# Performance work log

Measured on AMD Instinct MI355X. Metric: run time of the kernel, lower is better.

Reference implementation:

```python
import jax, jax.numpy as jnp
import numpy as np

OBS_DIM, ACT_DIM = 512, 32
H1, H2 = 1024, 1024
BATCH = 4096
LOG2PI = float(np.log(2.0 * np.pi))


def setup_inputs() -> dict:
    key = jax.random.key(0)
    ks = jax.random.split(key, 9)
    def uinit(k, shape, fan_in):
        b = 1.0 / np.sqrt(fan_in)
        return jax.random.uniform(k, shape, jnp.float32, -b, b)
    return {
        "obs": jax.random.normal(ks[0], (BATCH, OBS_DIM), jnp.float32),
        "act": jax.random.normal(ks[1], (BATCH, ACT_DIM), jnp.float32),
        # stacked per-head weights: [act_dim, in, out]
        "W1": uinit(ks[2], (ACT_DIM, OBS_DIM, H1), OBS_DIM),
        "b1": uinit(ks[3], (ACT_DIM, H1), OBS_DIM),
        "W2": uinit(ks[4], (ACT_DIM, H1, H2), H1),
        "b2": uinit(ks[5], (ACT_DIM, H2), H1),
        "W3": uinit(ks[6], (ACT_DIM, H2), H2),   # out dim 1, squeezed
        "b3": uinit(ks[7], (ACT_DIM,), H2),
        "log_std": jnp.full((ACT_DIM,), -0.5, jnp.float32),
    }


def reference(obs, act, W1, b1, W2, b2, W3, b3, log_std):
    # act_dim decoupled 3-layer MLPs as batched GEMMs over the head axis 'a'
    x = jnp.tanh(jnp.einsum('bo,aoh->bah', obs, W1) + b1)          # [B, A, H1]
    x = jnp.tanh(jnp.einsum('bah,ahk->bak', x, W2) + b2)           # [B, A, H2]
    mu = jnp.einsum('bak,ak->ba', x, W3) + b3                      # [B, A]
    # diagonal Normal log_prob(act).sum(-1)
    z = (act - mu) * jnp.exp(-log_std)
    logp = jnp.sum(-0.5 * (z * z + LOG2PI) - log_std, axis=-1)     # [B]
    return (mu, logp)
```

## Files before the change

### kernel.cpp

```cpp
#include <hip/hip_runtime.h>
#include <hip/hip_bf16.h>

typedef unsigned short u16;
typedef __bf16 bf16x8 __attribute__((ext_vector_type(8)));
typedef float f32x4 __attribute__((ext_vector_type(4)));

#define LOG2PI_F 1.8378770664093453f

__device__ __forceinline__ u16 f2bf(float f) {
  union { __hip_bfloat16 h; u16 u; } cvt;
  cvt.h = __float2bfloat16(f);
  return cvt.u;
}

__device__ __forceinline__ float fast_tanh(float x) {
  float e = __expf(2.0f * x);
  return 1.0f - 2.0f * __builtin_amdgcn_rcpf(e + 1.0f);
}

__device__ __forceinline__ void load_lds16(const void* g, void* l) {
  __builtin_amdgcn_global_load_lds(
      (const __attribute__((address_space(1))) void*)g,
      (__attribute__((address_space(3))) void*)l,
      16, 0, 0);
}

__global__ void cvt_f32_bf16(const float* __restrict__ in, u16* __restrict__ out, int n4) {
  int i = blockIdx.x * blockDim.x + threadIdx.x;
  int stride = gridDim.x * blockDim.x;
  for (int j = i; j < n4; j += stride) {
    float4 v = reinterpret_cast<const float4*>(in)[j];
    ushort4 o;
    o.x = f2bf(v.x); o.y = f2bf(v.y); o.z = f2bf(v.z); o.w = f2bf(v.w);
    reinterpret_cast<ushort4*>(out)[j] = o;
  }
}

__global__ void transpose_cvt(const float* __restrict__ W, u16* __restrict__ Wt,
                              int K, int N) {
  __shared__ u16 t[64][66];
  const int a = blockIdx.z;
  const int n0 = blockIdx.x * 64, k0 = blockIdx.y * 64;
  const float* Wh = W + (size_t)a * K * N;
  u16* Wth = Wt + (size_t)a * N * K;
  const int tid = threadIdx.x;
#pragma unroll
  for (int j = 0; j < 16; ++j) {
    int idx = j * 256 + tid;
    int r = idx >> 6, c = idx & 63;
    t[r][c] = f2bf(Wh[(size_t)(k0 + r) * N + n0 + c]);
  }
  __syncthreads();
#pragma unroll
  for (int j = 0; j < 16; ++j) {
    int idx = j * 256 + tid;
    int r = idx >> 6, c = idx & 63;
    Wth[(size_t)(n0 + r) * K + k0 + c] = t[c][r];
  }
}

template <int MODE>
__global__ __launch_bounds__(256, 2) void gemm_heads(
    const u16* __restrict__ A, long aHeadStride,
    const u16* __restrict__ Bt,
    const float* __restrict__ bias,
    int M, int N, int K, int gridN,
    u16* __restrict__ outBf,
    const float* __restrict__ W3,
    float* __restrict__ muAcc) {
  __shared__ __align__(16) u16 As[128 * 64];
  __shared__ __align__(16) u16 Bs[128 * 64];

  const int tid = threadIdx.x;
  const int l = tid & 63;
  const int w = tid >> 6;
  const int wm = w >> 1, wn = w & 1;
  const int lh = l & 15, lg = l >> 4;

  const int cpx = gridDim.x >> 3;
  const int bid = (blockIdx.x & 7) * cpx + (blockIdx.x >> 3);
  const int bph = (M >> 7) * gridN;
  const int head = bid / bph;
  const int rem = bid % bph;
  const int m0 = (rem / gridN) << 7;
  const int n0 = (rem % gridN) << 7;

  const u16* Ah = A + (size_t)head * (size_t)aHeadStride;
  const u16* Bh = Bt + (size_t)head * (size_t)N * (size_t)K;

  f32x4 acc[4][4] = {};

  for (int kt = 0; kt < K; kt += 64) {
#pragma unroll
    for (int i = 0; i < 4; ++i) {
      const int c = i * 256 + tid;
      const int row = c >> 3, j = c & 7;
      const int js = j ^ (row & 7);
      load_lds16(Ah + (size_t)(m0 + row) * K + kt + js * 8, &As[c * 8]);
    }
#pragma unroll
    for (int i = 0; i < 4; ++i) {
      const int c = i * 256 + tid;
      const int row = c >> 3, j = c & 7;
      const int js = j ^ (row & 7);
      load_lds16(Bh + (size_t)(n0 + row) * K + kt + js * 8, &Bs[c * 8]);
    }
    __syncthreads();

#pragma unroll
    for (int ks = 0; ks < 2; ++ks) {
      bf16x8 af[4], bfr[4];
#pragma unroll
      for (int mf = 0; mf < 4; ++mf) {
        const int row = wm * 64 + mf * 16 + lh;
        const int j = (ks * 4 + lg) ^ (lh & 7);
        af[mf] = *reinterpret_cast<const bf16x8*>(&As[row * 64 + j * 8]);
      }
#pragma unroll
      for (int nf = 0; nf < 4; ++nf) {
        const int row = wn * 64 + nf * 16 + lh;
        const int j = (ks * 4 + lg) ^ (lh & 7);
        bfr[nf] = *reinterpret_cast<const bf16x8*>(&Bs[row * 64 + j * 8]);
      }
#pragma unroll
      for (int mf = 0; mf < 4; ++mf)
#pragma unroll
        for (int nf = 0; nf < 4; ++nf)
          acc[mf][nf] = __builtin_amdgcn_mfma_f32_16x16x32_bf16(
              af[mf], bfr[nf], acc[mf][nf], 0, 0, 0);
    }
    __syncthreads();
  }

  if (MODE == 1) {
    u16* Oh = outBf + (size_t)head * (size_t)M * (size_t)N;
#pragma unroll
    for (int mf = 0; mf < 4; ++mf) {
#pragma unroll
      for (int r = 0; r < 4; ++r) {
        const int row = m0 + wm * 64 + mf * 16 + lg * 4 + r;
#pragma unroll
        for (int nf = 0; nf < 4; ++nf) {
          const int col = n0 + wn * 64 + nf * 16 + lh;
          float v = acc[mf][nf][r] + bias[head * N + col];
          Oh[(size_t)row * N + col] = f2bf(fast_tanh(v));
        }
      }
    }
  } else {
#pragma unroll
    for (int mf = 0; mf < 4; ++mf) {
#pragma unroll
      for (int r = 0; r < 4; ++r) {
        const int row = m0 + wm * 64 + mf * 16 + lg * 4 + r;
        float p = 0.f;
#pragma unroll
        for (int nf = 0; nf < 4; ++nf) {
          const int col = n0 + wn * 64 + nf * 16 + lh;
          float v = acc[mf][nf][r] + bias[head * N + col];
          p += fast_tanh(v) * W3[head * N + col];
        }
        p += __shfl_xor(p, 1);
        p += __shfl_xor(p, 2);
        p += __shfl_xor(p, 4);
        p += __shfl_xor(p, 8);
        if (lh == 0) atomicAdd(&muAcc[(size_t)row * 32 + head], p);
      }
    }
  }
}

__global__ void finalize_kernel(const float* __restrict__ muAcc,
                                const float* __restrict__ b3,
                                const float* __restrict__ lstd,
                                const float* __restrict__ act,
                                float* __restrict__ out, int M) {
  int b = blockIdx.x * 256 + threadIdx.x;
  if (b >= M) return;
  float lp = 0.f;
#pragma unroll
  for (int a = 0; a < 32; ++a) {
    float mu = muAcc[(size_t)b * 32 + a] + b3[a];
    out[(size_t)b * 32 + a] = mu;
    float ls = lstd[a];
    float z = (act[(size_t)b * 32 + a] - mu) * __expf(-ls);
    lp += -0.5f * (z * z + LOG2PI_F) - ls;
  }
  out[(size_t)M * 32 + b] = lp;
}

extern "C" void kernel_launch(void* const* d_in, const int* in_sizes, int n_in,
                              void* d_out, int out_size, void* d_ws, size_t ws_size,
                              hipStream_t stream) {
  const float* obs = (const float*)d_in[0];
  const float* act = (const float*)d_in[1];
  const float* W1 = (const float*)d_in[2];
  const float* b1 = (const float*)d_in[3];
  const float* W2 = (const float*)d_in[4];
  const float* b2 = (const float*)d_in[5];
  const float* W3 = (const float*)d_in[6];
  const float* b3 = (const float*)d_in[7];
  const float* lstd = (const float*)d_in[8];

  constexpr int B = 4096, OBS = 512, A = 32, H1 = 1024, H2 = 1024;

  u16* obs_bf = (u16*)d_ws;
  u16* W1t = obs_bf + (size_t)B * OBS;
  u16* W2t = W1t + (size_t)A * H1 * OBS;
  u16* x1 = W2t + (size_t)A * H2 * H1;
  float* muAcc = (float*)(x1 + (size_t)A * B * H1);
  float* out = (float*)d_out;

  hipMemsetAsync(muAcc, 0, (size_t)B * A * sizeof(float), stream);

  cvt_f32_bf16<<<1024, 256, 0, stream>>>(obs, obs_bf, B * OBS / 4);
  transpose_cvt<<<dim3(H1 / 64, OBS / 64, A), 256, 0, stream>>>(W1, W1t, OBS, H1);
  transpose_cvt<<<dim3(H2 / 64, H1 / 64, A), 256, 0, stream>>>(W2, W2t, H1, H2);

  gemm_heads<1><<<(B / 128) * (H1 / 128) * A, 256, 0, stream>>>(
      obs_bf, 0L, W1t, b1, B, H1, OBS, H1 / 128, x1, nullptr, nullptr);

  gemm_heads<2><<<(B / 128) * (H2 / 128) * A, 256, 0, stream>>>(
      x1, (long)B * H1, W2t, b2, B, H2, H1, H2 / 128, nullptr, W3, muAcc);

  finalize_kernel<<<B / 256, 256, 0, stream>>>(muAcc, b3, lstd, act, out, B);
}
```

Before: 723.6 us.

## Use 256x256 tiles with double-buffered LDS prefetch and vectorize weight transpose

The per-head GEMM moves from 128x128 tiles with 256 threads to 256x256 tiles with 1024 threads (16 waves). Each K-slice is staged into one of two LDS buffers, and loads for step t+2 are issued while the current slice is computed, using explicit vmcnt waits and barriers in place of __syncthreads. The goal is to hide global-to-LDS latency and roughly halve redundant operand traffic per output. The weight transpose/convert kernel now uses float4 loads and 16-byte stores with a padded tile. The cost is 128KB of LDS per block, which limits occupancy to a single block per CU, and the hand-placed waitcnt logic is fragile.

```diff
diff --git a/kernel.cpp b/kernel.cpp
--- a/kernel.cpp
+++ b/kernel.cpp
@@ -2,7 +2,9 @@
 #include <hip/hip_bf16.h>
 
 typedef unsigned short u16;
+typedef unsigned int u32;
 typedef __bf16 bf16x8 __attribute__((ext_vector_type(8)));
+typedef u16 u16x8 __attribute__((ext_vector_type(8)));
 typedef float f32x4 __attribute__((ext_vector_type(4)));
 
 #define LOG2PI_F 1.8378770664093453f
@@ -38,29 +40,42 @@
 
 __global__ void transpose_cvt(const float* __restrict__ W, u16* __restrict__ Wt,
                               int K, int N) {
-  __shared__ u16 t[64][66];
+  __shared__ u16 t[64][70];
   const int a = blockIdx.z;
   const int n0 = blockIdx.x * 64, k0 = blockIdx.y * 64;
   const float* Wh = W + (size_t)a * K * N;
   u16* Wth = Wt + (size_t)a * N * K;
   const int tid = threadIdx.x;
-#pragma unroll
-  for (int j = 0; j < 16; ++j) {
-    int idx = j * 256 + tid;
-    int r = idx >> 6, c = idx & 63;
-    t[r][c] = f2bf(Wh[(size_t)(k0 + r) * N + n0 + c]);
+
+  const int kk = tid >> 3, nn = (tid & 7) * 8;
+#pragma unroll
+  for (int p = 0; p < 2; ++p) {
+    const int k = kk + p * 32;
+    const float4* src =
+        reinterpret_cast<const float4*>(&Wh[(size_t)(k0 + k) * N + n0 + nn]);
+    float4 v0 = src[0];
+    float4 v1 = src[1];
+    u32* dst = reinterpret_cast<u32*>(&t[k][nn]);
+    dst[0] = (u32)f2bf(v0.x) | ((u32)f2bf(v0.y) << 16);
+    dst[1] = (u32)f2bf(v0.z) | ((u32)f2bf(v0.w) << 16);
+    dst[2] = (u32)f2bf(v1.x) | ((u32)f2bf(v1.y) << 16);
+    dst[3] = (u32)f2bf(v1.z) | ((u32)f2bf(v1.w) << 16);
   }
   __syncthreads();
-#pragma unroll
-  for (int j = 0; j < 16; ++j) {
-    int idx = j * 256 + tid;
-    int r = idx >> 6, c = idx & 63;
-    Wth[(size_t)(n0 + r) * K + k0 + c] = t[c][r];
+
+  const int kk8 = (tid & 7) * 8;
+#pragma unroll
+  for (int p = 0; p < 2; ++p) {
+    const int n = (tid >> 3) + p * 32;
+    u16x8 v;
+#pragma unroll
+    for (int q = 0; q < 8; ++q) v[q] = t[kk8 + q][n];
+    *reinterpret_cast<u16x8*>(&Wth[(size_t)(n0 + n) * K + k0 + kk8]) = v;
   }
 }
 
 template <int MODE>
-__global__ __launch_bounds__(256, 2) void gemm_heads(
+__global__ __launch_bounds__(1024, 4) void gemm256(
     const u16* __restrict__ A, long aHeadStride,
     const u16* __restrict__ Bt,
     const float* __restrict__ bias,
@@ -68,48 +83,63 @@
     u16* __restrict__ outBf,
     const float* __restrict__ W3,
     float* __restrict__ muAcc) {
-  __shared__ __align__(16) u16 As[128 * 64];
-  __shared__ __align__(16) u16 Bs[128 * 64];
+  __shared__ __align__(16) u16 lds[2][2][256 * 64];
 
   const int tid = threadIdx.x;
-  const int l = tid & 63;
-  const int w = tid >> 6;
-  const int wm = w >> 1, wn = w & 1;
+  const int w = tid >> 6, l = tid & 63;
+  const int wm = w >> 2, wn = w & 3;
   const int lh = l & 15, lg = l >> 4;
 
   const int cpx = gridDim.x >> 3;
   const int bid = (blockIdx.x & 7) * cpx + (blockIdx.x >> 3);
-  const int bph = (M >> 7) * gridN;
+  const int bph = (M >> 8) * gridN;
   const int head = bid / bph;
   const int rem = bid % bph;
-  const int m0 = (rem / gridN) << 7;
-  const int n0 = (rem % gridN) << 7;
+  const int m0 = (rem / gridN) << 8;
+  const int n0 = (rem % gridN) << 8;
 
   const u16* Ah = A + (size_t)head * (size_t)aHeadStride;
   const u16* Bh = Bt + (size_t)head * (size_t)N * (size_t)K;
 
+  auto stage = [&](int buf, int kt) {
+#pragma unroll
+    for (int i = 0; i < 2; ++i) {
+      int c = i * 1024 + tid;
+      int row = c >> 3, j = c & 7;
+      int js = j ^ (row & 7);
+      load_lds16(Ah + (size_t)(m0 + row) * K + kt + js * 8, &lds[buf][0][c * 8]);
+    }
+#pragma unroll
+    for (int i = 0; i < 2; ++i) {
+      int c = i * 1024 + tid;
+      int row = c >> 3, j = c & 7;
+      int js = j ^ (row & 7);
+      load_lds16(Bh + (size_t)(n0 + row) * K + kt + js * 8, &lds[buf][1][c * 8]);
+    }
+  };
+
   f32x4 acc[4][4] = {};
-
-  for (int kt = 0; kt < K; kt += 64) {
-#pragma unroll
-    for (int i = 0; i < 4; ++i) {
-      const int c = i * 256 + tid;
-      const int row = c >> 3, j = c & 7;
-      const int js = j ^ (row & 7);
-      load_lds16(Ah + (size_t)(m0 + row) * K + kt + js * 8, &As[c * 8]);
-    }
-#pragma unroll
-    for (int i = 0; i < 4; ++i) {
-      const int c = i * 256 + tid;
-      const int row = c >> 3, j = c & 7;
-      const int js = j ^ (row & 7);
-      load_lds16(Bh + (size_t)(n0 + row) * K + kt + js * 8, &Bs[c * 8]);
-    }
-    __syncthreads();
+  const int NT = K >> 6;
+
+  stage(0, 0);
+  stage(1, 64);
+  asm volatile("s_waitcnt vmcnt(4)" ::: "memory");
+  __builtin_amdgcn_sched_barrier(0);
+  __builtin_amdgcn_s_barrier();
+
+  for (int t = 0; t < NT; ++t) {
+    const u16* As = lds[t & 1][0];
+    const u16* Bs = lds[t & 1][1];
 
 #pragma unroll
     for (int ks = 0; ks < 2; ++ks) {
       bf16x8 af[4], bfr[4];
+#pragma unroll
+      for (int nf = 0; nf < 4; ++nf) {
+        const int row = wn * 64 + nf * 16 + lh;
+        const int j = (ks * 4 + lg) ^ (lh & 7);
+        bfr[nf] = *reinterpret_cast<const bf16x8*>(&Bs[row * 64 + j * 8]);
+      }
 #pragma unroll
       for (int mf = 0; mf < 4; ++mf) {
         const int row = wm * 64 + mf * 16 + lh;
@@ -117,19 +147,23 @@
         af[mf] = *reinterpret_cast<const bf16x8*>(&As[row * 64 + j * 8]);
       }
 #pragma unroll
-      for (int nf = 0; nf < 4; ++nf) {
-        const int row = wn * 64 + nf * 16 + lh;
-        const int j = (ks * 4 + lg) ^ (lh & 7);
-        bfr[nf] = *reinterpret_cast<const bf16x8*>(&Bs[row * 64 + j * 8]);
-      }
-#pragma unroll
       for (int mf = 0; mf < 4; ++mf)
 #pragma unroll
         for (int nf = 0; nf < 4; ++nf)
           acc[mf][nf] = __builtin_amdgcn_mfma_f32_16x16x32_bf16(
               af[mf], bfr[nf], acc[mf][nf], 0, 0, 0);
     }
-    __syncthreads();
+
+    __builtin_amdgcn_s_barrier();
+    __builtin_amdgcn_sched_barrier(0);
+    if (t + 2 < NT) {
+      stage(t & 1, (t + 2) << 6);
+      asm volatile("s_waitcnt vmcnt(4)" ::: "memory");
+    } else {
+      asm volatile("s_waitcnt vmcnt(0)" ::: "memory");
+    }
+    __builtin_amdgcn_sched_barrier(0);
+    __builtin_amdgcn_s_barrier();
   }
 
   if (MODE == 1) {
@@ -217,11 +251,11 @@
   transpose_cvt<<<dim3(H1 / 64, OBS / 64, A), 256, 0, stream>>>(W1, W1t, OBS, H1);
   transpose_cvt<<<dim3(H2 / 64, H1 / 64, A), 256, 0, stream>>>(W2, W2t, H1, H2);
 
-  gemm_heads<1><<<(B / 128) * (H1 / 128) * A, 256, 0, stream>>>(
-      obs_bf, 0L, W1t, b1, B, H1, OBS, H1 / 128, x1, nullptr, nullptr);
-
-  gemm_heads<2><<<(B / 128) * (H2 / 128) * A, 256, 0, stream>>>(
-      x1, (long)B * H1, W2t, b2, B, H2, H1, H2 / 128, nullptr, W3, muAcc);
+  gemm256<1><<<(B / 256) * (H1 / 256) * A, 1024, 0, stream>>>(
+      obs_bf, 0L, W1t, b1, B, H1, OBS, H1 / 256, x1, nullptr, nullptr);
+
+  gemm256<2><<<(B / 256) * (H2 / 256) * A, 1024, 0, stream>>>(
+      x1, (long)B * H1, W2t, b2, B, H2, H1, H2 / 256, nullptr, W3, muAcc);
 
   finalize_kernel<<<B / 256, 256, 0, stream>>>(muAcc, b3, lstd, act, out, B);
 }
```

Result: slower. 755.0 us (+4.4%).
